# Optimization experiments

Measured on AMD Instinct MI355X. Metric: run time of the kernel, lower is better.

Reference implementation:

```python
import jax, jax.numpy as jnp
import numpy as np

GRID_SIZE = 5
SPLINE_ORDER = 3


def b_splines(x):
    """Cox-de Boor B-spline bases. x: [N, in] -> [N, in, GRID_SIZE+SPLINE_ORDER]."""
    k = SPLINE_ORDER
    h = 2.0 / GRID_SIZE  # grid range [-1, 1]
    grid = jnp.arange(-k, GRID_SIZE + k + 1, dtype=x.dtype) * h - 1.0  # [G+2k+1]
    xe = x[..., None]  # [N, in, 1]
    b = ((xe >= grid[:-1]) & (xe < grid[1:])).astype(x.dtype)
    for j in range(1, k + 1):
        b = ((xe - grid[:-(j + 1)]) / (grid[j:-1] - grid[:-(j + 1)]) * b[..., :-1]
             + (grid[j + 1:] - xe) / (grid[j + 1:] - grid[1:-j]) * b[..., 1:])
    return b  # [N, in, G+k]


def kan_linear(x, base_w, spline_w):
    """efficient-KAN KANLinear: silu base branch + spline branch.
    x: [N, in], base_w: [out, in], spline_w: [out, in, G+k] -> [N, out]."""
    base = jnp.einsum('ni,oi->no', jax.nn.silu(x), base_w)
    spline = jnp.einsum('nig,oig->no', b_splines(x), spline_w)
    return base + spline


def setup_inputs() -> dict:
    key = jax.random.key(0)
    ks = jax.random.split(key, 8)
    C, R, G = 128, 8, GRID_SIZE + SPLINE_ORDER  # in_channels, reduced, n_bases
    B, H, W, D = 2, 64, 64, 64
    s = 0.1  # keep spline weights in a sane init range
    return {
        'x': jax.random.normal(ks[0], (B, C, H, W, D), dtype=jnp.float32),
        'ck1_base': jax.random.normal(ks[1], (R, C), dtype=jnp.float32) * s,
        'ck1_spline': jax.random.normal(ks[2], (R, C, G), dtype=jnp.float32) * s,
        'ck2_base': jax.random.normal(ks[3], (C, R), dtype=jnp.float32) * s,
        'ck2_spline': jax.random.normal(ks[4], (C, R, G), dtype=jnp.float32) * s,
        'conv_w': jax.random.normal(ks[5], (C,), dtype=jnp.float32) * 0.1,
        'sk_base': jax.random.normal(ks[6], (1, 1), dtype=jnp.float32),
        'sk_spline': jax.random.normal(ks[7], (1, 1, G), dtype=jnp.float32),
    }


def reference(x, ck1_base, ck1_spline, ck2_base, ck2_spline, conv_w, sk_base, sk_spline):
    B, C, H, W, D = x.shape
    # channel attention: avg/max pool -> KAN -> ReLU -> KAN, shared weights
    y_avg = jnp.mean(x, axis=(2, 3, 4))  # [B, C]
    y_max = jnp.max(x, axis=(2, 3, 4))   # [B, C]

    def channel_mlp(y):
        h1 = jax.nn.relu(kan_linear(y, ck1_base, ck1_spline))
        return kan_linear(h1, ck2_base, ck2_spline)

    channel_att = jax.nn.sigmoid(channel_mlp(y_avg) + channel_mlp(y_max))
    x_channel = x * channel_att[:, :, None, None, None]

    # spatial attention: 1x1x1 conv (C->1, no bias) then per-voxel 1->1 KAN
    y_spatial = jnp.einsum('bchwd,c->bhwd', x_channel, conv_w)
    y_flat = y_spatial.reshape(-1, 1)  # [B*H*W*D, 1]
    spatial_att = jax.nn.sigmoid(kan_linear(y_flat, sk_base, sk_spline))
    spatial_att = spatial_att.reshape(B, 1, H, W, D)
    return x_channel * spatial_att
```

## Files before the change

kernel.cpp:

```cpp
#include <hip/hip_runtime.h>
#include <math.h>

#define HWD 262144
#define C_CH 128
#define B_N 2

__device__ __forceinline__ float sigmoidf_(float v) {
    return 1.0f / (1.0f + expf(-v));
}

__device__ __forceinline__ void bspline8(float x, float* bs) {
    float g[12];
#pragma unroll
    for (int i = 0; i < 12; ++i) g[i] = (float)(i - 3) * 0.4f - 1.0f;
    float b[11];
#pragma unroll
    for (int t = 0; t < 11; ++t) b[t] = (x >= g[t] && x < g[t + 1]) ? 1.0f : 0.0f;
#pragma unroll
    for (int j = 1; j <= 3; ++j) {
#pragma unroll
        for (int t = 0; t + j < 11; ++t) {
            b[t] = (x - g[t]) / (g[t + j] - g[t]) * b[t]
                 + (g[t + j + 1] - x) / (g[t + j + 1] - g[t + 1]) * b[t + 1];
        }
    }
#pragma unroll
    for (int t = 0; t < 8; ++t) bs[t] = b[t];
}

__global__ __launch_bounds__(1024) void k1_pool(const float* __restrict__ x,
                                                float* __restrict__ ws) {
    int bid = blockIdx.x;
    const float4* xp = (const float4*)(x + (size_t)bid * HWD);
    int tid = threadIdx.x;
    float s = 0.0f, m = -INFINITY;
#pragma unroll 4
    for (int i = 0; i < 64; ++i) {
        float4 v = xp[(size_t)i * 1024 + tid];
        s += (v.x + v.y) + (v.z + v.w);
        m = fmaxf(m, fmaxf(fmaxf(v.x, v.y), fmaxf(v.z, v.w)));
    }
#pragma unroll
    for (int off = 32; off > 0; off >>= 1) {
        s += __shfl_xor(s, off, 64);
        m = fmaxf(m, __shfl_xor(m, off, 64));
    }
    __shared__ float ssum[16], smax[16];
    int wave = tid >> 6, lane = tid & 63;
    if (lane == 0) { ssum[wave] = s; smax[wave] = m; }
    __syncthreads();
    if (tid == 0) {
        float S = 0.0f, M = -INFINITY;
#pragma unroll
        for (int w = 0; w < 16; ++w) { S += ssum[w]; M = fmaxf(M, smax[w]); }
        ws[bid]       = S / (float)HWD;
        ws[256 + bid] = M;
    }
}

__global__ __launch_bounds__(512) void k2_catt(const float* ws_in,
                                               const float* __restrict__ ck1_base,
                                               const float* __restrict__ ck1_spline,
                                               const float* __restrict__ ck2_base,
                                               const float* __restrict__ ck2_spline,
                                               const float* __restrict__ conv_w,
                                               float* ws_out) {
    __shared__ float part[512 * 8];
    __shared__ float h1silu[32];
    __shared__ float h1bs[32][8];
    __shared__ float out2[512];
    int t = threadIdx.x;
    {
        int ysel = t >> 8, b = (t >> 7) & 1, i = t & 127;
        float v = ws_in[ysel * 256 + b * 128 + i];
        float sv = v * sigmoidf_(v);
        float bs[8];
        bspline8(v, bs);
#pragma unroll
        for (int r = 0; r < 8; ++r) {
            float acc = sv * ck1_base[r * 128 + i];
#pragma unroll
            for (int g = 0; g < 8; ++g)
                acc += bs[g] * ck1_spline[(r * 128 + i) * 8 + g];
            part[t * 8 + r] = acc;
        }
    }
    __syncthreads();
    if (t < 32) {
        int ysel = t >> 4, b = (t >> 3) & 1, r = t & 7;
        int tb = ysel * 256 + b * 128;
        float acc = 0.0f;
        for (int i = 0; i < 128; ++i) acc += part[(tb + i) * 8 + r];
        float h = fmaxf(acc, 0.0f);
        h1silu[t] = h * sigmoidf_(h);
        bspline8(h, h1bs[t]);
    }
    __syncthreads();
    {
        int ysel = t >> 8, b = (t >> 7) & 1, o = t & 127;
        float acc = 0.0f;
#pragma unroll
        for (int r = 0; r < 8; ++r) {
            int hidx = ysel * 16 + b * 8 + r;
            acc += h1silu[hidx] * ck2_base[o * 8 + r];
#pragma unroll
            for (int g = 0; g < 8; ++g)
                acc += h1bs[hidx][g] * ck2_spline[(o * 8 + r) * 8 + g];
        }
        out2[t] = acc;
    }
    __syncthreads();
    if (t < 256) {
        int o = t & 127;
        float catt = sigmoidf_(out2[t] + out2[256 + t]);
        ws_out[512 + t] = catt;
        ws_out[768 + t] = catt * conv_w[o];
    }
}

__global__ __launch_bounds__(256) void k3_main(const float* __restrict__ x,
                                               const float* __restrict__ ws,
                                               const float* __restrict__ sk_base,
                                               const float* __restrict__ sk_spline,
                                               float* __restrict__ out) {
    __shared__ __align__(16) float xs[C_CH * 64];
    __shared__ float partial[256];
    __shared__ __align__(16) float satt[64];
    __shared__ float catts[C_CH];
    __shared__ float w2s[C_CH];
    int tid = threadIdx.x;
    int bid = blockIdx.x;
    int b = bid >> 12;
    int v0 = (bid & 4095) << 6;
    if (tid < 128) {
        catts[tid] = ws[512 + b * 128 + tid];
        w2s[tid]   = ws[768 + b * 128 + tid];
    }
    const float* xb = x + (size_t)b * C_CH * HWD + v0;
#pragma unroll
    for (int m = 0; m < 8; ++m) {
        int f = m * 256 + tid;
        int c = f >> 4;
        int j = f & 15;
        float4 v = *(const float4*)(xb + (size_t)c * HWD + j * 4);
        *(float4*)&xs[c * 64 + j * 4] = v;
    }
    __syncthreads();
    {
        int v = tid & 63, q = tid >> 6;
        float acc = 0.0f;
#pragma unroll
        for (int cc = 0; cc < 32; ++cc) {
            int c = q * 32 + cc;
            acc += xs[c * 64 + v] * w2s[c];
        }
        partial[tid] = acc;
    }
    __syncthreads();
    if (tid < 64) {
        float s = partial[tid] + partial[tid + 64] + partial[tid + 128] + partial[tid + 192];
        float bs[8];
        bspline8(s, bs);
        float a = s * sigmoidf_(s) * sk_base[0];
#pragma unroll
        for (int g = 0; g < 8; ++g) a += bs[g] * sk_spline[g];
        satt[tid] = sigmoidf_(a);
    }
    __syncthreads();
    float* ob = out + (size_t)b * C_CH * HWD + v0;
#pragma unroll
    for (int m = 0; m < 8; ++m) {
        int f = m * 256 + tid;
        int c = f >> 4;
        int j = f & 15;
        float4 v = *(float4*)&xs[c * 64 + j * 4];
        float4 sa = *(float4*)&satt[j * 4];
        float ca = catts[c];
        float4 o;
        o.x = v.x * ca * sa.x;
        o.y = v.y * ca * sa.y;
        o.z = v.z * ca * sa.z;
        o.w = v.w * ca * sa.w;
        *(float4*)(ob + (size_t)c * HWD + j * 4) = o;
    }
}

extern "C" void kernel_launch(void* const* d_in, const int* in_sizes, int n_in,
                              void* d_out, int out_size, void* d_ws, size_t ws_size,
                              hipStream_t stream) {
    const float* x          = (const float*)d_in[0];
    const float* ck1_base   = (const float*)d_in[1];
    const float* ck1_spline = (const float*)d_in[2];
    const float* ck2_base   = (const float*)d_in[3];
    const float* ck2_spline = (const float*)d_in[4];
    const float* conv_w     = (const float*)d_in[5];
    const float* sk_base    = (const float*)d_in[6];
    const float* sk_spline  = (const float*)d_in[7];
    float* out = (float*)d_out;
    float* ws  = (float*)d_ws;

    k1_pool<<<B_N * C_CH, 1024, 0, stream>>>(x, ws);
    k2_catt<<<1, 512, 0, stream>>>(ws, ck1_base, ck1_spline, ck2_base, ck2_spline,
                                   conv_w, ws);
    k3_main<<<B_N * (HWD / 64), 256, 0, stream>>>(x, ws, sk_base, sk_spline, out);
}
```

Before: 509.0 us.

## Split pooling across more blocks and reverse main-kernel order for L2 reuse

```diff
diff --git a/kernel.cpp b/kernel.cpp
--- a/kernel.cpp
+++ b/kernel.cpp
@@ -28,15 +28,16 @@
     for (int t = 0; t < 8; ++t) bs[t] = b[t];
 }
 
-__global__ __launch_bounds__(1024) void k1_pool(const float* __restrict__ x,
-                                                float* __restrict__ ws) {
+__global__ __launch_bounds__(256) void k1_pool(const float* __restrict__ x,
+                                               float* __restrict__ ws) {
     int bid = blockIdx.x;
-    const float4* xp = (const float4*)(x + (size_t)bid * HWD);
+    int bc = bid >> 2, chunk = bid & 3;
+    const float4* xp = (const float4*)(x + (size_t)bc * HWD + (size_t)chunk * 65536);
     int tid = threadIdx.x;
     float s = 0.0f, m = -INFINITY;
-#pragma unroll 4
+#pragma unroll 8
     for (int i = 0; i < 64; ++i) {
-        float4 v = xp[(size_t)i * 1024 + tid];
+        float4 v = xp[i * 256 + tid];
         s += (v.x + v.y) + (v.z + v.w);
         m = fmaxf(m, fmaxf(fmaxf(v.x, v.y), fmaxf(v.z, v.w)));
     }
@@ -45,16 +46,13 @@
         s += __shfl_xor(s, off, 64);
         m = fmaxf(m, __shfl_xor(m, off, 64));
     }
-    __shared__ float ssum[16], smax[16];
-    int wave = tid >> 6, lane = tid & 63;
-    if (lane == 0) { ssum[wave] = s; smax[wave] = m; }
+    __shared__ float ss[4], sm[4];
+    int wave = tid >> 6;
+    if ((tid & 63) == 0) { ss[wave] = s; sm[wave] = m; }
     __syncthreads();
     if (tid == 0) {
-        float S = 0.0f, M = -INFINITY;
-#pragma unroll
-        for (int w = 0; w < 16; ++w) { S += ssum[w]; M = fmaxf(M, smax[w]); }
-        ws[bid]       = S / (float)HWD;
-        ws[256 + bid] = M;
+        ws[bid]        = (ss[0] + ss[1]) + (ss[2] + ss[3]);
+        ws[1024 + bid] = fmaxf(fmaxf(sm[0], sm[1]), fmaxf(sm[2], sm[3]));
     }
 }
 
@@ -65,14 +63,22 @@
                                                const float* __restrict__ ck2_spline,
                                                const float* __restrict__ conv_w,
                                                float* ws_out) {
+    __shared__ float y[512];
     __shared__ float part[512 * 8];
     __shared__ float h1silu[32];
     __shared__ float h1bs[32][8];
     __shared__ float out2[512];
     int t = threadIdx.x;
+    if (t < 256) {
+        y[t] = (ws_in[t * 4] + ws_in[t * 4 + 1] + ws_in[t * 4 + 2] + ws_in[t * 4 + 3])
+               * (1.0f / (float)HWD);
+        y[256 + t] = fmaxf(fmaxf(ws_in[1024 + t * 4],     ws_in[1024 + t * 4 + 1]),
+                           fmaxf(ws_in[1024 + t * 4 + 2], ws_in[1024 + t * 4 + 3]));
+    }
+    __syncthreads();
     {
-        int ysel = t >> 8, b = (t >> 7) & 1, i = t & 127;
-        float v = ws_in[ysel * 256 + b * 128 + i];
+        int i = t & 127;
+        float v = y[t];
         float sv = v * sigmoidf_(v);
         float bs[8];
         bspline8(v, bs);
@@ -113,67 +119,66 @@
     if (t < 256) {
         int o = t & 127;
         float catt = sigmoidf_(out2[t] + out2[256 + t]);
-        ws_out[512 + t] = catt;
-        ws_out[768 + t] = catt * conv_w[o];
-    }
-}
-
-__global__ __launch_bounds__(256) void k3_main(const float* __restrict__ x,
-                                               const float* __restrict__ ws,
-                                               const float* __restrict__ sk_base,
-                                               const float* __restrict__ sk_spline,
-                                               float* __restrict__ out) {
-    __shared__ __align__(16) float xs[C_CH * 64];
-    __shared__ float partial[256];
-    __shared__ __align__(16) float satt[64];
+        ws_out[2048 + t] = catt;
+        ws_out[2304 + t] = catt * conv_w[o];
+    }
+}
+
+__global__ __launch_bounds__(1024) void k3_main(const float* __restrict__ x,
+                                                const float* __restrict__ ws,
+                                                const float* __restrict__ sk_base,
+                                                const float* __restrict__ sk_spline,
+                                                float* __restrict__ out) {
+    __shared__ __align__(16) float xs[C_CH * 256];
+    __shared__ float partial[1024];
+    __shared__ __align__(16) float satt[256];
     __shared__ float catts[C_CH];
     __shared__ float w2s[C_CH];
     int tid = threadIdx.x;
-    int bid = blockIdx.x;
-    int b = bid >> 12;
-    int v0 = (bid & 4095) << 6;
+    int g = 2047 - (int)blockIdx.x;
+    int b = g >> 10;
+    int v0 = (g & 1023) << 8;
     if (tid < 128) {
-        catts[tid] = ws[512 + b * 128 + tid];
-        w2s[tid]   = ws[768 + b * 128 + tid];
+        catts[tid] = ws[2048 + b * 128 + tid];
+        w2s[tid]   = ws[2304 + b * 128 + tid];
     }
     const float* xb = x + (size_t)b * C_CH * HWD + v0;
 #pragma unroll
     for (int m = 0; m < 8; ++m) {
-        int f = m * 256 + tid;
-        int c = f >> 4;
-        int j = f & 15;
-        float4 v = *(const float4*)(xb + (size_t)c * HWD + j * 4);
-        *(float4*)&xs[c * 64 + j * 4] = v;
+        int f = m * 1024 + tid;
+        int c = f >> 6;
+        int j = f & 63;
+        *(float4*)&xs[c * 256 + j * 4] = *(const float4*)(xb + (size_t)c * HWD + j * 4);
     }
     __syncthreads();
     {
-        int v = tid & 63, q = tid >> 6;
+        int v = tid & 255, q = tid >> 8;
         float acc = 0.0f;
 #pragma unroll
         for (int cc = 0; cc < 32; ++cc) {
             int c = q * 32 + cc;
-            acc += xs[c * 64 + v] * w2s[c];
+            acc += xs[c * 256 + v] * w2s[c];
         }
         partial[tid] = acc;
     }
     __syncthreads();
-    if (tid < 64) {
-        float s = partial[tid] + partial[tid + 64] + partial[tid + 128] + partial[tid + 192];
+    if (tid < 256) {
+        float s = partial[tid] + partial[tid + 256] + partial[tid + 512] + partial[tid + 768];
         float bs[8];
         bspline8(s, bs);
         float a = s * sigmoidf_(s) * sk_base[0];
 #pragma unroll
-        for (int g = 0; g < 8; ++g) a += bs[g] * sk_spline[g];
+        for (int g2 = 0; g2 < 8; ++g2) a += bs[g2] * sk_spline[g2];
         satt[tid] = sigmoidf_(a);
     }
     __syncthreads();
     float* ob = out + (size_t)b * C_CH * HWD + v0;
 #pragma unroll
     for (int m = 0; m < 8; ++m) {
-        int f = m * 256 + tid;
-        int c = f >> 4;
-        int j = f & 15;
-        float4 v = *(float4*)&xs[c * 64 + j * 4];
+        int f = m * 1024 + tid;
+        int c = f >> 6;
+        int j = f & 63;
+        float4 v = *(float4*)&xs[c * 256 + j * 4];
         float4 sa = *(float4*)&satt[j * 4];
         float ca = catts[c];
         float4 o;
@@ -199,8 +204,8 @@
     float* out = (float*)d_out;
     float* ws  = (float*)d_ws;
 
-    k1_pool<<<B_N * C_CH, 1024, 0, stream>>>(x, ws);
+    k1_pool<<<1024, 256, 0, stream>>>(x, ws);
     k2_catt<<<1, 512, 0, stream>>>(ws, ck1_base, ck1_spline, ck2_base, ck2_spline,
                                    conv_w, ws);
-    k3_main<<<B_N * (HWD / 64), 256, 0, stream>>>(x, ws, sk_base, sk_spline, out);
-}
+    k3_main<<<B_N * (HWD / 256), 1024, 0, stream>>>(x, ws, sk_base, sk_spline, out);
+}
```

Result: slower. 521.8 us (+2.5%).
